# Performance work log

Measured on AMD Instinct MI355X. Metric: run time of the kernel, lower is better.

## Reference

```python
import jax, jax.numpy as jnp
import numpy as np

B_SZ, N, D = 256, 64, 32

def setup_inputs() -> dict:
    key = jax.random.key(0)
    k1, k2, k3 = jax.random.split(key, 3)
    A = jax.random.normal(k1, (B_SZ, N, N, D), dtype=jnp.float32)
    B = jax.random.normal(k2, (B_SZ, N, N, D), dtype=jnp.float32)
    # ragged per-graph node counts in [1, N]
    counts = jax.random.randint(k3, (B_SZ,), 1, N + 1, dtype=jnp.int32)
    return {"A": A, "B": B, "counts": counts}


def _pair_mask(counts):
    # node validity mask (b, n) -> tuple (i, j) mask (b, n, n)
    nodemask = jnp.arange(N)[None, :] < counts[:, None]
    return nodemask[:, :, None] & nodemask[:, None, :]


def reference(A, B, counts):
    mask = _pair_mask(counts)  # (b, n, n) bool, shared by A, B and tarX
    m = mask[..., None]
    Af = jnp.where(m, A, 0.0)  # MaskedTensor.fill_masked(0)
    Bf = jnp.where(m, B, 0.0)
    # mamamm with dim1=2, dim2=1 (after batch offset): contract A's dim 2
    # with B's dim 1, dense channel dim d elementwise-broadcast.
    out = jnp.einsum('bikd,bkjd->bijd', Af, Bf)
    # output masked by tarX.mask
    return jnp.where(m, out, 0.0)
```

## Files before the change

kernel.cpp:

```cpp
#include <hip/hip_runtime.h>


#define BATCH 256
#define NN 64
#define ND 32
#define BSTRIDE (NN * NN * ND)
#define RSTRIDE (NN * ND)

__global__ __launch_bounds__(512, 4) void mp_kernel(
    const float* __restrict__ A,
    const float* __restrict__ B,
    const int* __restrict__ counts,
    float* __restrict__ out)
{
    const int b  = blockIdx.x & (BATCH - 1);
    const int ic = blockIdx.x >> 8;
    const int i0 = ic << 3;
    const int c  = counts[b];
    const int tid = (int)threadIdx.x;
    const int d  = tid & 31;
    const int jg = tid >> 5;
    const int jb = jg << 2;

    const size_t base = (size_t)b * BSTRIDE;
    float* __restrict__ Ob = out + base + (size_t)i0 * RSTRIDE + (size_t)jb * ND + d;

    if (i0 >= c) {
        #pragma unroll
        for (int ii = 0; ii < 8; ++ii)
            #pragma unroll
            for (int jj = 0; jj < 4; ++jj)
                Ob[(size_t)ii * RSTRIDE + jj * ND] = 0.0f;
        return;
    }

    const float* __restrict__ Ai = A + base + (size_t)i0 * RSTRIDE + d;
    const float* __restrict__ Bb = B + base + (size_t)jb * ND + d;

    float acc[8][4];
    #pragma unroll
    for (int ii = 0; ii < 8; ++ii)
        #pragma unroll
        for (int jj = 0; jj < 4; ++jj)
            acc[ii][jj] = 0.0f;

    const bool waveActive = (((tid >> 6) << 3) < c);

    if (waveActive) {
        #pragma unroll 2
        for (int k = 0; k < c; ++k) {
            float av[8];
            #pragma unroll
            for (int ii = 0; ii < 8; ++ii)
                av[ii] = Ai[(size_t)ii * RSTRIDE + k * ND];
            float bv[4];
            #pragma unroll
            for (int jj = 0; jj < 4; ++jj)
                bv[jj] = Bb[(size_t)k * RSTRIDE + jj * ND];
            #pragma unroll
            for (int ii = 0; ii < 8; ++ii)
                #pragma unroll
                for (int jj = 0; jj < 4; ++jj)
                    acc[ii][jj] = fmaf(av[ii], bv[jj], acc[ii][jj]);
        }
    }

    #pragma unroll
    for (int ii = 0; ii < 8; ++ii) {
        const int i = i0 + ii;
        const bool iv = (i < c);
        #pragma unroll
        for (int jj = 0; jj < 4; ++jj) {
            const bool v = iv && ((jb + jj) < c);
            Ob[(size_t)ii * RSTRIDE + jj * ND] = v ? acc[ii][jj] : 0.0f;
        }
    }
}

extern "C" void kernel_launch(void* const* d_in, const int* in_sizes, int n_in,
                              void* d_out, int out_size, void* d_ws, size_t ws_size,
                              hipStream_t stream)
{
    const float* A      = (const float*)d_in[0];
    const float* B      = (const float*)d_in[1];
    const int*   counts = (const int*)d_in[2];
    float* out = (float*)d_out;

    mp_kernel<<<dim3(BATCH * 8), dim3(512), 0, stream>>>(A, B, counts, out);
}
```

Measured before the change: 98.36 us.

## Retile mp_kernel to float4 channel vectors with 4x2 i-j register tiles

Each thread now owns 4 consecutive channels, 2 j columns and 4 i rows, and reads A and B with float4 loads. Outputs are written with float4 stores. The block size drops to 256 threads and the i-chunk to 4 rows, which doubles the grid size. The aim is fewer load and store instructions per FMA and wider memory transactions. In exchange, B is re-read by twice as many i-chunk blocks, and the loop holds fewer FMAs per A row.

```diff
diff --git a/kernel.cpp b/kernel.cpp
--- a/kernel.cpp
+++ b/kernel.cpp
@@ -6,8 +6,9 @@
 #define ND 32
 #define BSTRIDE (NN * NN * ND)
 #define RSTRIDE (NN * ND)
+#define ICHUNK 4
 
-__global__ __launch_bounds__(512, 4) void mp_kernel(
+__global__ __launch_bounds__(256, 4) void mp_kernel(
     const float* __restrict__ A,
     const float* __restrict__ B,
     const int* __restrict__ counts,
@@ -15,64 +16,75 @@
 {
     const int b  = blockIdx.x & (BATCH - 1);
     const int ic = blockIdx.x >> 8;
-    const int i0 = ic << 3;
+    const int i0 = ic * ICHUNK;
     const int c  = counts[b];
     const int tid = (int)threadIdx.x;
-    const int d  = tid & 31;
-    const int jg = tid >> 5;
-    const int jb = jg << 2;
+    const int d4 = tid & 7;
+    const int jp = tid >> 3;
+    const int j0 = jp << 1;
 
     const size_t base = (size_t)b * BSTRIDE;
-    float* __restrict__ Ob = out + base + (size_t)i0 * RSTRIDE + (size_t)jb * ND + d;
+    float* __restrict__ Ob = out + base + (size_t)i0 * RSTRIDE + (size_t)j0 * ND + d4 * 4;
 
     if (i0 >= c) {
+        const float4 z = make_float4(0.f, 0.f, 0.f, 0.f);
         #pragma unroll
-        for (int ii = 0; ii < 8; ++ii)
+        for (int ii = 0; ii < ICHUNK; ++ii)
             #pragma unroll
-            for (int jj = 0; jj < 4; ++jj)
-                Ob[(size_t)ii * RSTRIDE + jj * ND] = 0.0f;
+            for (int jj = 0; jj < 2; ++jj)
+                *reinterpret_cast<float4*>(Ob + (size_t)ii * RSTRIDE + jj * ND) = z;
         return;
     }
 
-    const float* __restrict__ Ai = A + base + (size_t)i0 * RSTRIDE + d;
-    const float* __restrict__ Bb = B + base + (size_t)jb * ND + d;
+    const float4* __restrict__ A4 =
+        reinterpret_cast<const float4*>(A + base + (size_t)i0 * RSTRIDE) + d4;
+    const float4* __restrict__ B4 =
+        reinterpret_cast<const float4*>(B + base + (size_t)j0 * ND) + d4;
 
-    float acc[8][4];
+    float acc[ICHUNK][2][4];
     #pragma unroll
-    for (int ii = 0; ii < 8; ++ii)
+    for (int ii = 0; ii < ICHUNK; ++ii)
         #pragma unroll
-        for (int jj = 0; jj < 4; ++jj)
-            acc[ii][jj] = 0.0f;
+        for (int jj = 0; jj < 2; ++jj)
+            #pragma unroll
+            for (int dd = 0; dd < 4; ++dd)
+                acc[ii][jj][dd] = 0.0f;
 
-    const bool waveActive = (((tid >> 6) << 3) < c);
+    const bool waveActive = (((tid >> 6) << 4) < c);
 
     if (waveActive) {
         #pragma unroll 2
         for (int k = 0; k < c; ++k) {
-            float av[8];
+            float4 bv0 = B4[(size_t)k * (RSTRIDE / 4)];
+            float4 bv1 = B4[(size_t)k * (RSTRIDE / 4) + (ND / 4)];
+            float4 av[ICHUNK];
             #pragma unroll
-            for (int ii = 0; ii < 8; ++ii)
-                av[ii] = Ai[(size_t)ii * RSTRIDE + k * ND];
-            float bv[4];
+            for (int ii = 0; ii < ICHUNK; ++ii)
+                av[ii] = A4[(size_t)ii * (RSTRIDE / 4) + (size_t)k * (ND / 4)];
             #pragma unroll
-            for (int jj = 0; jj < 4; ++jj)
-                bv[jj] = Bb[(size_t)k * RSTRIDE + jj * ND];
-            #pragma unroll
-            for (int ii = 0; ii < 8; ++ii)
-                #pragma unroll
-                for (int jj = 0; jj < 4; ++jj)
-                    acc[ii][jj] = fmaf(av[ii], bv[jj], acc[ii][jj]);
+            for (int ii = 0; ii < ICHUNK; ++ii) {
+                acc[ii][0][0] = fmaf(av[ii].x, bv0.x, acc[ii][0][0]);
+                acc[ii][0][1] = fmaf(av[ii].y, bv0.y, acc[ii][0][1]);
+                acc[ii][0][2] = fmaf(av[ii].z, bv0.z, acc[ii][0][2]);
+                acc[ii][0][3] = fmaf(av[ii].w, bv0.w, acc[ii][0][3]);
+                acc[ii][1][0] = fmaf(av[ii].x, bv1.x, acc[ii][1][0]);
+                acc[ii][1][1] = fmaf(av[ii].y, bv1.y, acc[ii][1][1]);
+                acc[ii][1][2] = fmaf(av[ii].z, bv1.z, acc[ii][1][2]);
+                acc[ii][1][3] = fmaf(av[ii].w, bv1.w, acc[ii][1][3]);
+            }
         }
     }
 
     #pragma unroll
-    for (int ii = 0; ii < 8; ++ii) {
-        const int i = i0 + ii;
-        const bool iv = (i < c);
+    for (int ii = 0; ii < ICHUNK; ++ii) {
+        const bool iv = (i0 + ii) < c;
         #pragma unroll
-        for (int jj = 0; jj < 4; ++jj) {
-            const bool v = iv && ((jb + jj) < c);
-            Ob[(size_t)ii * RSTRIDE + jj * ND] = v ? acc[ii][jj] : 0.0f;
+        for (int jj = 0; jj < 2; ++jj) {
+            const bool v = iv && ((j0 + jj) < c);
+            const float4 o = v ? make_float4(acc[ii][jj][0], acc[ii][jj][1],
+                                             acc[ii][jj][2], acc[ii][jj][3])
+                               : make_float4(0.f, 0.f, 0.f, 0.f);
+            *reinterpret_cast<float4*>(Ob + (size_t)ii * RSTRIDE + jj * ND) = o;
         }
     }
 }
@@ -86,5 +98,5 @@
     const int*   counts = (const int*)d_in[2];
     float* out = (float*)d_out;
 
-    mp_kernel<<<dim3(BATCH * 8), dim3(512), 0, stream>>>(A, B, counts, out);
+    mp_kernel<<<dim3(BATCH * (NN / ICHUNK)), dim3(256), 0, stream>>>(A, B, counts, out);
 }
```

New measurement: 133.0 us. 1.35x slower.

## Sort work items by descending graph size via prologue kernel for load balance

Applied to the files above, without the earlier changes.

Adds a single-block prologue kernel that builds a counting-sort histogram over (batch, i-chunk) work items keyed by node count. It writes a permutation into the workspace so the heavy blocks with the largest counts are dispatched first and zero-fill-only blocks run last. This targets tail imbalance from ragged counts. It also lowers the launch_bounds occupancy hint from 4 to 2. In exchange it pays for an extra kernel launch, a serial prefix scan, and one indirect load per block, and it relies on a workspace being available.

```diff
diff --git a/kernel.cpp b/kernel.cpp
--- a/kernel.cpp
+++ b/kernel.cpp
@@ -6,15 +6,49 @@
 #define ND 32
 #define BSTRIDE (NN * NN * ND)
 #define RSTRIDE (NN * ND)
+#define ICHUNK 8
+#define NITEMS (BATCH * (NN / ICHUNK))
 
-__global__ __launch_bounds__(512, 4) void mp_kernel(
-    const float* __restrict__ A,
-    const float* __restrict__ B,
-    const int* __restrict__ counts,
-    float* __restrict__ out)
+__global__ __launch_bounds__(512) void mp_prologue(
+    const int* __restrict__ counts, int* __restrict__ items)
 {
-    const int b  = blockIdx.x & (BATCH - 1);
-    const int ic = blockIdx.x >> 8;
+    __shared__ int cLds[BATCH];
+    __shared__ int hist[NN + 1];
+    __shared__ int offs[NN + 1];
+    const int tid = (int)threadIdx.x;
+
+    if (tid <= NN) hist[tid] = 0;
+    for (int b = tid; b < BATCH; b += 512) cLds[b] = counts[b];
+    __syncthreads();
+
+    for (int w = tid; w < NITEMS; w += 512) {
+        const int b = w >> 3, ic = w & 7;
+        const int c = cLds[b];
+        const int key = (ic * ICHUNK < c) ? (NN - c) : NN;
+        atomicAdd(&hist[key], 1);
+    }
+    __syncthreads();
+
+    if (tid == 0) {
+        int acc = 0;
+        for (int k = 0; k <= NN; ++k) { offs[k] = acc; acc += hist[k]; }
+    }
+    __syncthreads();
+
+    for (int w = tid; w < NITEMS; w += 512) {
+        const int b = w >> 3, ic = w & 7;
+        const int c = cLds[b];
+        const int key = (ic * ICHUNK < c) ? (NN - c) : NN;
+        const int pos = atomicAdd(&offs[key], 1);
+        items[pos] = w;
+    }
+}
+
+__device__ __forceinline__ void mp_body(
+    int b, int ic,
+    const float* __restrict__ A, const float* __restrict__ B,
+    const int* __restrict__ counts, float* __restrict__ out)
+{
     const int i0 = ic << 3;
     const int c  = counts[b];
     const int tid = (int)threadIdx.x;
@@ -27,7 +61,7 @@
 
     if (i0 >= c) {
         #pragma unroll
-        for (int ii = 0; ii < 8; ++ii)
+        for (int ii = 0; ii < ICHUNK; ++ii)
             #pragma unroll
             for (int jj = 0; jj < 4; ++jj)
                 Ob[(size_t)ii * RSTRIDE + jj * ND] = 0.0f;
@@ -37,9 +71,9 @@
     const float* __restrict__ Ai = A + base + (size_t)i0 * RSTRIDE + d;
     const float* __restrict__ Bb = B + base + (size_t)jb * ND + d;
 
-    float acc[8][4];
+    float acc[ICHUNK][4];
     #pragma unroll
-    for (int ii = 0; ii < 8; ++ii)
+    for (int ii = 0; ii < ICHUNK; ++ii)
         #pragma unroll
         for (int jj = 0; jj < 4; ++jj)
             acc[ii][jj] = 0.0f;
@@ -49,16 +83,16 @@
     if (waveActive) {
         #pragma unroll 2
         for (int k = 0; k < c; ++k) {
-            float av[8];
+            float av[ICHUNK];
             #pragma unroll
-            for (int ii = 0; ii < 8; ++ii)
+            for (int ii = 0; ii < ICHUNK; ++ii)
                 av[ii] = Ai[(size_t)ii * RSTRIDE + k * ND];
             float bv[4];
             #pragma unroll
             for (int jj = 0; jj < 4; ++jj)
                 bv[jj] = Bb[(size_t)k * RSTRIDE + jj * ND];
             #pragma unroll
-            for (int ii = 0; ii < 8; ++ii)
+            for (int ii = 0; ii < ICHUNK; ++ii)
                 #pragma unroll
                 for (int jj = 0; jj < 4; ++jj)
                     acc[ii][jj] = fmaf(av[ii], bv[jj], acc[ii][jj]);
@@ -66,15 +100,30 @@
     }
 
     #pragma unroll
-    for (int ii = 0; ii < 8; ++ii) {
-        const int i = i0 + ii;
-        const bool iv = (i < c);
+    for (int ii = 0; ii < ICHUNK; ++ii) {
+        const bool iv = (i0 + ii) < c;
         #pragma unroll
         for (int jj = 0; jj < 4; ++jj) {
             const bool v = iv && ((jb + jj) < c);
             Ob[(size_t)ii * RSTRIDE + jj * ND] = v ? acc[ii][jj] : 0.0f;
         }
     }
+}
+
+__global__ __launch_bounds__(512, 2) void mp_kernel_sorted(
+    const float* __restrict__ A, const float* __restrict__ B,
+    const int* __restrict__ counts, float* __restrict__ out,
+    const int* __restrict__ items)
+{
+    const int w = items[blockIdx.x];
+    mp_body(w >> 3, w & 7, A, B, counts, out);
+}
+
+__global__ __launch_bounds__(512, 2) void mp_kernel_direct(
+    const float* __restrict__ A, const float* __restrict__ B,
+    const int* __restrict__ counts, float* __restrict__ out)
+{
+    mp_body(blockIdx.x & (BATCH - 1), blockIdx.x >> 8, A, B, counts, out);
 }
 
 extern "C" void kernel_launch(void* const* d_in, const int* in_sizes, int n_in,
@@ -86,5 +135,11 @@
     const int*   counts = (const int*)d_in[2];
     float* out = (float*)d_out;
 
-    mp_kernel<<<dim3(BATCH * 8), dim3(512), 0, stream>>>(A, B, counts, out);
+    if (ws_size >= NITEMS * sizeof(int)) {
+        int* items = (int*)d_ws;
+        mp_prologue<<<dim3(1), dim3(512), 0, stream>>>(counts, items);
+        mp_kernel_sorted<<<dim3(NITEMS), dim3(512), 0, stream>>>(A, B, counts, out, items);
+    } else {
+        mp_kernel_direct<<<dim3(NITEMS), dim3(512), 0, stream>>>(A, B, counts, out);
+    }
 }
```

Measured after the change: 97.36 us. No clear change (-1.0%).
